# Kernel optimization log

Measured on AMD Instinct MI355X. Metric: run time of the kernel, lower is better.

The kernel has to match this reference:

```python
import jax, jax.numpy as jnp
import numpy as np

B, S, D = 256, 256, 1024
P = D // 2  # proj_dim default = input_dim / 2
NUM_HIDDEN = 2
EPS = 1e-7  # K.epsilon()
INIT_SCALE = 0.05  # keras 'uniform' init


def setup_inputs() -> dict:
    key = jax.random.key(0)
    ks = jax.random.split(key, 8)
    x = jax.random.normal(ks[0], (B, S, D), dtype=jnp.float32)
    mask = jax.random.randint(ks[1], (B, S), 0, 2).astype(bool)
    u = lambda k, shp: jax.random.uniform(k, shp, jnp.float32, -INIT_SCALE, INIT_SCALE)
    proj_head = u(ks[2], (D, P))
    proj_prep = u(ks[3], (D, P))
    proj_child = u(ks[4], (D, P))
    hidden_layers = u(ks[5], (NUM_HIDDEN, P, P))
    scorer = u(ks[6], (P,))
    return {"x": x, "proj_head": proj_head, "proj_prep": proj_prep,
            "proj_child": proj_child, "hidden_layers": hidden_layers,
            "scorer": scorer, "mask": mask}


def reference(x, proj_head, proj_prep, proj_child, hidden_layers, scorer, mask):
    # x: [B, S, D]; last two timesteps are preposition and child noun.
    head_enc = x[:, :-2, :]          # [B, S-2, D]
    prep_enc = x[:, -2, :]           # [B, D]
    child_enc = x[:, -1, :]          # [B, D]

    head_proj = jnp.einsum('bsd,dp->bsp', head_enc, proj_head)      # [B, S-2, P]
    prep_proj = (prep_enc @ proj_prep)[:, None, :]                  # [B, 1, P]
    child_proj = (child_enc @ proj_child)[:, None, :]               # [B, 1, P]

    # composition_type == 'HPCT'
    composed = jnp.tanh(head_proj + prep_proj + child_proj)         # [B, S-2, P]

    for i in range(hidden_layers.shape[0]):  # small fixed layer count
        composed = jnp.tanh(jnp.einsum('bsp,pq->bsq', composed, hidden_layers[i]))

    scores = jnp.einsum('bsp,p->bs', composed, scorer)              # [B, S-2]

    # masked exp-normalization (as in the original Keras code)
    exp_scores = jnp.exp(scores)
    head_mask = mask[:, :-2]
    masked_exp = jnp.where(head_mask, exp_scores, 0.0)
    exp_sum = jnp.sum(masked_exp, axis=1, keepdims=True) + EPS
    return masked_exp / exp_sum
```

## Files before the change

kernel.cpp:

```cpp
#include <hip/hip_runtime.h>
#include <hip/hip_bf16.h>
#include <stdint.h>

#define B_ 256
#define S_ 256
#define D_ 1024
#define P_ 512
#define SH 254
#define M_ (B_*SH)
#define EPSF 1e-7f

typedef __attribute__((ext_vector_type(8))) short short8v;
typedef __attribute__((ext_vector_type(4))) float float4v;

__device__ inline short f2bf(float f) {
  __hip_bfloat16 h = __float2bfloat16(f);
  return *reinterpret_cast<short*>(&h);
}
__device__ inline float fast_tanh(float x) {
  float e = __expf(2.0f * x);
  return 1.0f - 2.0f * __builtin_amdgcn_rcpf(e + 1.0f);
}

__global__ void k_detect(const unsigned char* m, int* flag) {
  __shared__ int c0, c3;
  if (threadIdx.x == 0) { c0 = 0; c3 = 0; }
  __syncthreads();
  int f0 = 0, f3 = 0;
  for (int i = threadIdx.x; i < 4096; i += 256) {
    unsigned char v = m[i];
    if (v != 0) {
      if ((i & 3) == 0) f0 = 1;
      if ((i & 3) == 3) f3 = 1;
    }
  }
  if (f0) atomicOr(&c0, 1);
  if (f3) atomicOr(&c3, 1);
  __syncthreads();
  if (threadIdx.x == 0) {
    int f;
    if (c3 == 0) f = 0;
    else if (c0 != 0) f = 1;
    else f = 2;
    *flag = f;
  }
}

__global__ void k_trans_head(const float* w, short* out) {
  int idx = blockIdx.x * 256 + threadIdx.x;
  int n = idx & (P_ - 1);
  int k = idx >> 9;
  out[(k >> 5) * (P_*32) + n*32 + (k & 31)] = f2bf(w[k*P_ + n]);
}

__global__ void k_trans_hidden(const float* h, short* o0, short* o1) {
  int idx = blockIdx.x * 256 + threadIdx.x;
  int which = idx >> 18;
  int j = idx & ((P_*P_) - 1);
  int n = j & (P_ - 1);
  int k = j >> 9;
  short v = f2bf(h[which*(P_*P_) + k*P_ + n]);
  short* o = which ? o1 : o0;
  o[(k >> 5) * (P_*32) + n*32 + (k & 31)] = v;
}

__global__ void __launch_bounds__(512) k_pc(const float* __restrict__ x,
                                            const float* __restrict__ wp,
                                            const float* __restrict__ wc,
                                            float* __restrict__ pc) {
  __shared__ float xs[16][256];
  int bg = blockIdx.x >> 4, cs = blockIdx.x & 15;
  int t = threadIdx.x;
  int bloc = t >> 5, c = t & 31;
  int batch = bg * 16 + bloc;
  int col = cs * 32 + c;
  float acc = 0.f;
  #pragma unroll
  for (int half = 0; half < 2; half++) {
    const float* wsrc = half ? wc : wp;
    for (int kc = 0; kc < 4; kc++) {
      const float* xr = x + ((size_t)(batch * S_ + SH + half)) * D_ + kc*256 + c*8;
      float4 v0 = *(const float4*)(xr + 0);
      float4 v1 = *(const float4*)(xr + 4);
      __syncthreads();
      *(float4*)&xs[bloc][c*8 + 0] = v0;
      *(float4*)&xs[bloc][c*8 + 4] = v1;
      __syncthreads();
      const float* wv = wsrc + (size_t)(kc*256) * P_ + col;
      #pragma unroll 8
      for (int d = 0; d < 256; d++) {
        acc += xs[bloc][d] * wv[(size_t)d * P_];
      }
    }
  }
  pc[batch * P_ + col] = acc;
}

__global__ void __launch_bounds__(512, 2) k_main(
    const float* __restrict__ x, const short* __restrict__ wth,
    const short* __restrict__ h0t, const short* __restrict__ h1t,
    const float* __restrict__ scorer, const float* __restrict__ pc,
    float* __restrict__ scores)
{
  __shared__ __attribute__((aligned(16))) short As[2][64*136];
  __shared__ __attribute__((aligned(16))) short Cs[64*520];
  __shared__ float scorer_s[P_];
  __shared__ float score_s[64];

  const int tid  = threadIdx.x;
  const int lane = tid & 63;
  const int wn   = tid >> 6;
  const int l15  = lane & 15, quad = lane >> 4;
  const int rowbase = blockIdx.x * 64;

  scorer_s[tid] = scorer[tid];
  if (tid < 64) score_s[tid] = 0.f;

  const int arow = tid >> 3;
  const int akg  = (tid & 7) * 16;
  {
    int r0 = rowbase + arow;
    int ab = r0 / SH;
    int as_ = r0 - ab * SH;
    const float* aptr = x + ((size_t)(ab * S_ + as_)) * D_ + akg;

    float4 st0 = *(const float4*)(aptr + 0);
    float4 st1 = *(const float4*)(aptr + 4);
    float4 st2 = *(const float4*)(aptr + 8);
    float4 st3 = *(const float4*)(aptr + 12);
    short8v s0 = { f2bf(st0.x),f2bf(st0.y),f2bf(st0.z),f2bf(st0.w),
                   f2bf(st1.x),f2bf(st1.y),f2bf(st1.z),f2bf(st1.w) };
    short8v s1 = { f2bf(st2.x),f2bf(st2.y),f2bf(st2.z),f2bf(st2.w),
                   f2bf(st3.x),f2bf(st3.y),f2bf(st3.z),f2bf(st3.w) };
    *(short8v*)&As[0][arow*136 + akg]     = s0;
    *(short8v*)&As[0][arow*136 + akg + 8] = s1;
    __syncthreads();

    float4v acc[4][4];
    #pragma unroll
    for (int i = 0; i < 4; i++)
      #pragma unroll
      for (int j = 0; j < 4; j++) acc[i][j] = (float4v){0.f,0.f,0.f,0.f};

    const uint4* wb = (const uint4*)wth;

    for (int sc = 0; sc < 8; sc++) {
      const int cur = sc & 1;
      float4 n0, n1, n2, n3;
      if (sc < 7) {
        const float* p = aptr + (sc + 1) * 128;
        n0 = *(const float4*)(p + 0);
        n1 = *(const float4*)(p + 4);
        n2 = *(const float4*)(p + 8);
        n3 = *(const float4*)(p + 12);
      }
      #pragma unroll
      for (int c = 0; c < 4; c++) {
        const int kc = sc * 4 + c;
        short8v a[4];
        #pragma unroll
        for (int mt = 0; mt < 4; mt++)
          a[mt] = *(const short8v*)&As[cur][(mt*16 + l15)*136 + c*32 + quad*8];
        #pragma unroll
        for (int nt = 0; nt < 4; nt++) {
          uint4 bv = wb[(size_t)kc*2048 + (wn*64 + nt*16 + l15)*4 + quad];
          short8v bfr = *(short8v*)&bv;
          #pragma unroll
          for (int mt = 0; mt < 4; mt++)
            acc[mt][nt] = __builtin_amdgcn_mfma_f32_16x16x32_bf16(a[mt], bfr, acc[mt][nt], 0, 0, 0);
        }
      }
      if (sc < 7) {
        short8v w0 = { f2bf(n0.x),f2bf(n0.y),f2bf(n0.z),f2bf(n0.w),
                       f2bf(n1.x),f2bf(n1.y),f2bf(n1.z),f2bf(n1.w) };
        short8v w1 = { f2bf(n2.x),f2bf(n2.y),f2bf(n2.z),f2bf(n2.w),
                       f2bf(n3.x),f2bf(n3.y),f2bf(n3.z),f2bf(n3.w) };
        *(short8v*)&As[cur ^ 1][arow*136 + akg]     = w0;
        *(short8v*)&As[cur ^ 1][arow*136 + akg + 8] = w1;
      }
      __syncthreads();
    }

    #pragma unroll
    for (int mt = 0; mt < 4; mt++) {
      #pragma unroll
      for (int j = 0; j < 4; j++) {
        int rl = mt*16 + quad*4 + j;
        int rg = rowbase + rl;
        int bb = rg / SH;
        const float* pcb = pc + bb * P_;
        #pragma unroll
        for (int nt = 0; nt < 4; nt++) {
          int col = wn*64 + nt*16 + l15;
          float v = fast_tanh(acc[mt][nt][j] + pcb[col]);
          float o = __shfl_xor(v, 1, 64);
          unsigned hs = (unsigned short)f2bf(v);
          unsigned ho = (unsigned short)f2bf(o);
          if ((l15 & 1) == 0)
            *(unsigned*)&Cs[rl*520 + col] = hs | (ho << 16);
        }
      }
    }
    __syncthreads();

    #pragma unroll 1
    for (int stage = 0; stage < 2; stage++) {
      const uint4* hb = (const uint4*)(stage ? h1t : h0t);
      #pragma unroll
      for (int i = 0; i < 4; i++)
        #pragma unroll
        for (int j = 0; j < 4; j++) acc[i][j] = (float4v){0.f,0.f,0.f,0.f};
      #pragma unroll 4
      for (int kc = 0; kc < 16; kc++) {
        short8v a[4];
        #pragma unroll
        for (int mt = 0; mt < 4; mt++)
          a[mt] = *(const short8v*)&Cs[(mt*16 + l15)*520 + kc*32 + quad*8];
        #pragma unroll
        for (int nt = 0; nt < 4; nt++) {
          uint4 bv = hb[(size_t)kc*2048 + (wn*64 + nt*16 + l15)*4 + quad];
          short8v bfr = *(short8v*)&bv;
          #pragma unroll
          for (int mt = 0; mt < 4; mt++)
            acc[mt][nt] = __builtin_amdgcn_mfma_f32_16x16x32_bf16(a[mt], bfr, acc[mt][nt], 0, 0, 0);
        }
      }
      if (stage == 0) {
        __syncthreads();
        #pragma unroll
        for (int mt = 0; mt < 4; mt++) {
          #pragma unroll
          for (int j = 0; j < 4; j++) {
            int rl = mt*16 + quad*4 + j;
            #pragma unroll
            for (int nt = 0; nt < 4; nt++) {
              int col = wn*64 + nt*16 + l15;
              float v = fast_tanh(acc[mt][nt][j]);
              float o = __shfl_xor(v, 1, 64);
              unsigned hs = (unsigned short)f2bf(v);
              unsigned ho = (unsigned short)f2bf(o);
              if ((l15 & 1) == 0)
                *(unsigned*)&Cs[rl*520 + col] = hs | (ho << 16);
            }
          }
        }
        __syncthreads();
      }
    }

    #pragma unroll
    for (int mt = 0; mt < 4; mt++) {
      #pragma unroll
      for (int j = 0; j < 4; j++) {
        float part = 0.f;
        #pragma unroll
        for (int nt = 0; nt < 4; nt++) {
          int col = wn*64 + nt*16 + l15;
          part += fast_tanh(acc[mt][nt][j]) * scorer_s[col];
        }
        #pragma unroll
        for (int o = 1; o < 16; o <<= 1) part += __shfl_xor(part, o, 64);
        if (l15 == 0) atomicAdd(&score_s[mt*16 + quad*4 + j], part);
      }
    }
  }
  __syncthreads();
  if (tid < 64) scores[rowbase + tid] = __expf(score_s[tid]);
}

__global__ void __launch_bounds__(256) k_softmax(const float* __restrict__ scores,
                                                 const void* __restrict__ mask,
                                                 const int* __restrict__ flag,
                                                 float* __restrict__ out) {
  int b = blockIdx.x, t = threadIdx.x;
  int lane = t & 63, w = t >> 6;
  __shared__ float ps[4];
  float me = 0.f;
  bool valid = t < SH;
  if (valid) {
    float e = scores[b*SH + t];
    int f = *flag;
    bool mb;
    if (f == 1)      mb = ((const unsigned char*)mask)[b*S_ + t] != 0;
    else if (f == 2) mb = ((const float*)mask)[b*S_ + t] != 0.0f;
    else             mb = ((const int*)mask)[b*S_ + t] != 0;
    me = mb ? e : 0.f;
  }
  float v = me;
  for (int o = 1; o < 64; o <<= 1) v += __shfl_xor(v, o, 64);
  if (lane == 0) ps[w] = v;
  __syncthreads();
  float tot = ps[0] + ps[1] + ps[2] + ps[3] + EPSF;
  if (valid) out[b*SH + t] = me / tot;
}

extern "C" void kernel_launch(void* const* d_in, const int* in_sizes, int n_in,
                              void* d_out, int out_size, void* d_ws, size_t ws_size,
                              hipStream_t stream) {
  const float* x          = (const float*)d_in[0];
  const float* proj_head  = (const float*)d_in[1];
  const float* proj_prep  = (const float*)d_in[2];
  const float* proj_child = (const float*)d_in[3];
  const float* hidden     = (const float*)d_in[4];
  const float* scorer     = (const float*)d_in[5];
  const void*  mask       = d_in[6];
  float* out = (float*)d_out;
  char* ws = (char*)d_ws;

  int*   flag   = (int*)  (ws + 0);
  float* pc     = (float*)(ws + 256);
  short* wth    = (short*)(ws + 524544);
  short* h0t    = (short*)(ws + 1573120);
  short* h1t    = (short*)(ws + 2097408);
  float* scores = (float*)(ws + 2621696);

  k_detect<<<1, 256, 0, stream>>>((const unsigned char*)mask, flag);
  k_trans_head<<<2048, 256, 0, stream>>>(proj_head, wth);
  k_trans_hidden<<<2048, 256, 0, stream>>>(hidden, h0t, h1t);
  k_pc<<<256, 512, 0, stream>>>(x, proj_prep, proj_child, pc);
  k_main<<<1016, 512, 0, stream>>>(x, wth, h0t, h1t, scorer, pc, scores);
  k_softmax<<<256, 256, 0, stream>>>(scores, mask, flag, out);
}
```

Baseline: 745.5 us.

## Prefetch B fragments into registers, cache pc in LDS, drop score atomics

The main kernel now software-pipelines weight-fragment loads into two register buffers, prefetching the next pair of K-chunks while MFMAs run on the current pair. The prefetch carries across the stage boundary into the second hidden layer. The per-batch pc rows are staged in shared memory, and the LDS atomicAdd score reduction is replaced by per-wave slots summed at the end. The transpose kernels now write packed pairs of bf16 values. The double buffers add register pressure, which under the 512x2 launch bounds risks spills.

```diff
diff --git a/kernel.cpp b/kernel.cpp
--- a/kernel.cpp
+++ b/kernel.cpp
@@ -46,22 +46,33 @@
   }
 }
 
-__global__ void k_trans_head(const float* w, short* out) {
+__global__ void k_trans_head(const float* __restrict__ w, short* __restrict__ out) {
   int idx = blockIdx.x * 256 + threadIdx.x;
-  int n = idx & (P_ - 1);
-  int k = idx >> 9;
-  out[(k >> 5) * (P_*32) + n*32 + (k & 31)] = f2bf(w[k*P_ + n]);
-}
-
-__global__ void k_trans_hidden(const float* h, short* o0, short* o1) {
+  int kc  = idx >> 13;
+  int j   = idx & 8191;
+  int krp = j >> 9;
+  int n   = j & 511;
+  int k0  = kc * 32 + krp * 2;
+  unsigned lo = (unsigned short)f2bf(w[(size_t)k0 * P_ + n]);
+  unsigned hi = (unsigned short)f2bf(w[(size_t)(k0 + 1) * P_ + n]);
+  ((unsigned*)out)[kc * 8192 + n * 16 + krp] = lo | (hi << 16);
+}
+
+__global__ void k_trans_hidden(const float* __restrict__ h,
+                               short* __restrict__ o0, short* __restrict__ o1) {
   int idx = blockIdx.x * 256 + threadIdx.x;
-  int which = idx >> 18;
-  int j = idx & ((P_*P_) - 1);
-  int n = j & (P_ - 1);
-  int k = j >> 9;
-  short v = f2bf(h[which*(P_*P_) + k*P_ + n]);
-  short* o = which ? o1 : o0;
-  o[(k >> 5) * (P_*32) + n*32 + (k & 31)] = v;
+  int which = idx >> 17;
+  int j = idx & 131071;
+  int kc  = j >> 13;
+  int r   = j & 8191;
+  int krp = r >> 9;
+  int n   = r & 511;
+  const float* hs = h + (size_t)which * (P_*P_);
+  int k0 = kc * 32 + krp * 2;
+  unsigned lo = (unsigned short)f2bf(hs[(size_t)k0 * P_ + n]);
+  unsigned hi = (unsigned short)f2bf(hs[(size_t)(k0 + 1) * P_ + n]);
+  unsigned* o = (unsigned*)(which ? o1 : o0);
+  o[kc * 8192 + n * 16 + krp] = lo | (hi << 16);
 }
 
 __global__ void __launch_bounds__(512) k_pc(const float* __restrict__ x,
@@ -96,6 +107,41 @@
   pc[batch * P_ + col] = acc;
 }
 
+
+#define LB2(DST, BASE, KC0) do {                                    \
+  const uint4* _p = (BASE) + (size_t)(KC0)*2048 + bcol;             \
+  DST[0]=_p[0];    DST[1]=_p[64];      DST[2]=_p[128];  DST[3]=_p[192]; \
+  DST[4]=_p[2048]; DST[5]=_p[2048+64]; DST[6]=_p[2048+128]; DST[7]=_p[2048+192]; \
+} while(0)
+
+#define APAIR(CUR, CB, BUF) do {                                    \
+  _Pragma("unroll") for (int cc = 0; cc < 2; cc++) {                \
+    short8v a_[4];                                                  \
+    _Pragma("unroll") for (int mt = 0; mt < 4; mt++)                \
+      a_[mt] = *(const short8v*)&As[CUR][(mt*16 + l15)*136 + ((CB)+cc)*32 + quad*8]; \
+    _Pragma("unroll") for (int nt = 0; nt < 4; nt++) {              \
+      short8v bfr = *(short8v*)&BUF[cc*4 + nt];                     \
+      _Pragma("unroll") for (int mt = 0; mt < 4; mt++)              \
+        acc[mt][nt] = __builtin_amdgcn_mfma_f32_16x16x32_bf16(a_[mt], bfr, acc[mt][nt], 0, 0, 0); \
+    }                                                               \
+  }                                                                 \
+} while(0)
+
+#define S23(P, CURB, NXTB) do {                                     \
+  if ((P) < 7) { LB2(NXTB, hb, 2*(P)+2); }                          \
+  else if (stage == 0) { LB2(NXTB, h1v, 0); }                       \
+  _Pragma("unroll") for (int cc = 0; cc < 2; cc++) {                \
+    short8v a_[4];                                                  \
+    _Pragma("unroll") for (int mt = 0; mt < 4; mt++)                \
+      a_[mt] = *(const short8v*)&Cs[(mt*16 + l15)*520 + (2*(P)+cc)*32 + quad*8]; \
+    _Pragma("unroll") for (int nt = 0; nt < 4; nt++) {              \
+      short8v bfr = *(short8v*)&CURB[cc*4 + nt];                    \
+      _Pragma("unroll") for (int mt = 0; mt < 4; mt++)              \
+        acc[mt][nt] = __builtin_amdgcn_mfma_f32_16x16x32_bf16(a_[mt], bfr, acc[mt][nt], 0, 0, 0); \
+    }                                                               \
+  }                                                                 \
+} while(0)
+
 __global__ void __launch_bounds__(512, 2) k_main(
     const float* __restrict__ x, const short* __restrict__ wth,
     const short* __restrict__ h0t, const short* __restrict__ h1t,
@@ -105,7 +151,8 @@
   __shared__ __attribute__((aligned(16))) short As[2][64*136];
   __shared__ __attribute__((aligned(16))) short Cs[64*520];
   __shared__ float scorer_s[P_];
-  __shared__ float score_s[64];
+  __shared__ float pcs[2][P_];
+  __shared__ float score_ws[64][8];
 
   const int tid  = threadIdx.x;
   const int lane = tid & 63;
@@ -114,16 +161,27 @@
   const int rowbase = blockIdx.x * 64;
 
   scorer_s[tid] = scorer[tid];
-  if (tid < 64) score_s[tid] = 0.f;
+  const int bb0 = rowbase / SH;
+  const int bb1 = (rowbase + 63) / SH;
+  pcs[0][tid] = pc[bb0 * P_ + tid];
+  pcs[1][tid] = pc[bb1 * P_ + tid];
+  const int lim1 = (bb0 + 1) * SH;
 
   const int arow = tid >> 3;
   const int akg  = (tid & 7) * 16;
+  int r0 = rowbase + arow;
+  int ab = r0 / SH;
+  int as_ = r0 - ab * SH;
+  const float* aptr = x + ((size_t)(ab * S_ + as_)) * D_ + akg;
+
+  const uint4* wbv = (const uint4*)wth;
+  const uint4* h0v = (const uint4*)h0t;
+  const uint4* h1v = (const uint4*)h1t;
+  const int bcol = (wn*64 + l15)*4 + quad;
+
+  uint4 bA[8], bB[8];
+
   {
-    int r0 = rowbase + arow;
-    int ab = r0 / SH;
-    int as_ = r0 - ab * SH;
-    const float* aptr = x + ((size_t)(ab * S_ + as_)) * D_ + akg;
-
     float4 st0 = *(const float4*)(aptr + 0);
     float4 st1 = *(const float4*)(aptr + 4);
     float4 st2 = *(const float4*)(aptr + 8);
@@ -134,138 +192,122 @@
                    f2bf(st3.x),f2bf(st3.y),f2bf(st3.z),f2bf(st3.w) };
     *(short8v*)&As[0][arow*136 + akg]     = s0;
     *(short8v*)&As[0][arow*136 + akg + 8] = s1;
+  }
+  LB2(bA, wbv, 0);
+  __syncthreads();
+
+  float4v acc[4][4];
+  #pragma unroll
+  for (int i = 0; i < 4; i++)
+    #pragma unroll
+    for (int j = 0; j < 4; j++) acc[i][j] = (float4v){0.f,0.f,0.f,0.f};
+
+  for (int sc = 0; sc < 8; sc++) {
+    const int cur = sc & 1;
+    float4 n0, n1, n2, n3;
+    if (sc < 7) {
+      const float* p = aptr + (sc + 1) * 128;
+      n0 = *(const float4*)(p + 0);
+      n1 = *(const float4*)(p + 4);
+      n2 = *(const float4*)(p + 8);
+      n3 = *(const float4*)(p + 12);
+    }
+    LB2(bB, wbv, 4*sc + 2);
+    APAIR(cur, 0, bA);
+    if (sc < 7) { LB2(bA, wbv, 4*sc + 4); }
+    APAIR(cur, 2, bB);
+    if (sc < 7) {
+      short8v w0 = { f2bf(n0.x),f2bf(n0.y),f2bf(n0.z),f2bf(n0.w),
+                     f2bf(n1.x),f2bf(n1.y),f2bf(n1.z),f2bf(n1.w) };
+      short8v w1 = { f2bf(n2.x),f2bf(n2.y),f2bf(n2.z),f2bf(n2.w),
+                     f2bf(n3.x),f2bf(n3.y),f2bf(n3.z),f2bf(n3.w) };
+      *(short8v*)&As[cur ^ 1][arow*136 + akg]     = w0;
+      *(short8v*)&As[cur ^ 1][arow*136 + akg + 8] = w1;
+    }
     __syncthreads();
-
-    float4v acc[4][4];
+  }
+
+  LB2(bA, h0v, 0);
+
+  #pragma unroll
+  for (int mt = 0; mt < 4; mt++) {
+    #pragma unroll
+    for (int j = 0; j < 4; j++) {
+      int rl = mt*16 + quad*4 + j;
+      int rg = rowbase + rl;
+      const float* pcb = (rg >= lim1) ? pcs[1] : pcs[0];
+      #pragma unroll
+      for (int nt = 0; nt < 4; nt++) {
+        int col = wn*64 + nt*16 + l15;
+        float v = fast_tanh(acc[mt][nt][j] + pcb[col]);
+        float o = __shfl_xor(v, 1, 64);
+        unsigned hs = (unsigned short)f2bf(v);
+        unsigned ho = (unsigned short)f2bf(o);
+        if ((l15 & 1) == 0)
+          *(unsigned*)&Cs[rl*520 + col] = hs | (ho << 16);
+      }
+    }
+  }
+  __syncthreads();
+
+  #pragma unroll 1
+  for (int stage = 0; stage < 2; stage++) {
+    const uint4* hb = stage ? h1v : h0v;
     #pragma unroll
     for (int i = 0; i < 4; i++)
       #pragma unroll
       for (int j = 0; j < 4; j++) acc[i][j] = (float4v){0.f,0.f,0.f,0.f};
 
-    const uint4* wb = (const uint4*)wth;
-
-    for (int sc = 0; sc < 8; sc++) {
-      const int cur = sc & 1;
-      float4 n0, n1, n2, n3;
-      if (sc < 7) {
-        const float* p = aptr + (sc + 1) * 128;
-        n0 = *(const float4*)(p + 0);
-        n1 = *(const float4*)(p + 4);
-        n2 = *(const float4*)(p + 8);
-        n3 = *(const float4*)(p + 12);
-      }
-      #pragma unroll
-      for (int c = 0; c < 4; c++) {
-        const int kc = sc * 4 + c;
-        short8v a[4];
+    S23(0, bA, bB); S23(1, bB, bA);
+    S23(2, bA, bB); S23(3, bB, bA);
+    S23(4, bA, bB); S23(5, bB, bA);
+    S23(6, bA, bB); S23(7, bB, bA);
+
+    if (stage == 0) {
+      __syncthreads();
+      #pragma unroll
+      for (int mt = 0; mt < 4; mt++) {
         #pragma unroll
-        for (int mt = 0; mt < 4; mt++)
-          a[mt] = *(const short8v*)&As[cur][(mt*16 + l15)*136 + c*32 + quad*8];
-        #pragma unroll
-        for (int nt = 0; nt < 4; nt++) {
-          uint4 bv = wb[(size_t)kc*2048 + (wn*64 + nt*16 + l15)*4 + quad];
-          short8v bfr = *(short8v*)&bv;
+        for (int j = 0; j < 4; j++) {
+          int rl = mt*16 + quad*4 + j;
           #pragma unroll
-          for (int mt = 0; mt < 4; mt++)
-            acc[mt][nt] = __builtin_amdgcn_mfma_f32_16x16x32_bf16(a[mt], bfr, acc[mt][nt], 0, 0, 0);
+          for (int nt = 0; nt < 4; nt++) {
+            int col = wn*64 + nt*16 + l15;
+            float v = fast_tanh(acc[mt][nt][j]);
+            float o = __shfl_xor(v, 1, 64);
+            unsigned hs = (unsigned short)f2bf(v);
+            unsigned ho = (unsigned short)f2bf(o);
+            if ((l15 & 1) == 0)
+              *(unsigned*)&Cs[rl*520 + col] = hs | (ho << 16);
+          }
         }
       }
-      if (sc < 7) {
-        short8v w0 = { f2bf(n0.x),f2bf(n0.y),f2bf(n0.z),f2bf(n0.w),
-                       f2bf(n1.x),f2bf(n1.y),f2bf(n1.z),f2bf(n1.w) };
-        short8v w1 = { f2bf(n2.x),f2bf(n2.y),f2bf(n2.z),f2bf(n2.w),
-                       f2bf(n3.x),f2bf(n3.y),f2bf(n3.z),f2bf(n3.w) };
-        *(short8v*)&As[cur ^ 1][arow*136 + akg]     = w0;
-        *(short8v*)&As[cur ^ 1][arow*136 + akg + 8] = w1;
+      __syncthreads();
+    }
+  }
+
+  #pragma unroll
+  for (int mt = 0; mt < 4; mt++) {
+    #pragma unroll
+    for (int j = 0; j < 4; j++) {
+      float part = 0.f;
+      #pragma unroll
+      for (int nt = 0; nt < 4; nt++) {
+        int col = wn*64 + nt*16 + l15;
+        part += fast_tanh(acc[mt][nt][j]) * scorer_s[col];
       }
-      __syncthreads();
-    }
-
-    #pragma unroll
-    for (int mt = 0; mt < 4; mt++) {
-      #pragma unroll
-      for (int j = 0; j < 4; j++) {
-        int rl = mt*16 + quad*4 + j;
-        int rg = rowbase + rl;
-        int bb = rg / SH;
-        const float* pcb = pc + bb * P_;
-        #pragma unroll
-        for (int nt = 0; nt < 4; nt++) {
-          int col = wn*64 + nt*16 + l15;
-          float v = fast_tanh(acc[mt][nt][j] + pcb[col]);
-          float o = __shfl_xor(v, 1, 64);
-          unsigned hs = (unsigned short)f2bf(v);
-          unsigned ho = (unsigned short)f2bf(o);
-          if ((l15 & 1) == 0)
-            *(unsigned*)&Cs[rl*520 + col] = hs | (ho << 16);
-        }
-      }
-    }
-    __syncthreads();
-
-    #pragma unroll 1
-    for (int stage = 0; stage < 2; stage++) {
-      const uint4* hb = (const uint4*)(stage ? h1t : h0t);
-      #pragma unroll
-      for (int i = 0; i < 4; i++)
-        #pragma unroll
-        for (int j = 0; j < 4; j++) acc[i][j] = (float4v){0.f,0.f,0.f,0.f};
-      #pragma unroll 4
-      for (int kc = 0; kc < 16; kc++) {
-        short8v a[4];
-        #pragma unroll
-        for (int mt = 0; mt < 4; mt++)
-          a[mt] = *(const short8v*)&Cs[(mt*16 + l15)*520 + kc*32 + quad*8];
-        #pragma unroll
-        for (int nt = 0; nt < 4; nt++) {
-          uint4 bv = hb[(size_t)kc*2048 + (wn*64 + nt*16 + l15)*4 + quad];
-          short8v bfr = *(short8v*)&bv;
-          #pragma unroll
-          for (int mt = 0; mt < 4; mt++)
-            acc[mt][nt] = __builtin_amdgcn_mfma_f32_16x16x32_bf16(a[mt], bfr, acc[mt][nt], 0, 0, 0);
-        }
-      }
-      if (stage == 0) {
-        __syncthreads();
-        #pragma unroll
-        for (int mt = 0; mt < 4; mt++) {
-          #pragma unroll
-          for (int j = 0; j < 4; j++) {
-            int rl = mt*16 + quad*4 + j;
-            #pragma unroll
-            for (int nt = 0; nt < 4; nt++) {
-              int col = wn*64 + nt*16 + l15;
-              float v = fast_tanh(acc[mt][nt][j]);
-              float o = __shfl_xor(v, 1, 64);
-              unsigned hs = (unsigned short)f2bf(v);
-              unsigned ho = (unsigned short)f2bf(o);
-              if ((l15 & 1) == 0)
-                *(unsigned*)&Cs[rl*520 + col] = hs | (ho << 16);
-            }
-          }
-        }
-        __syncthreads();
-      }
-    }
-
-    #pragma unroll
-    for (int mt = 0; mt < 4; mt++) {
-      #pragma unroll
-      for (int j = 0; j < 4; j++) {
-        float part = 0.f;
-        #pragma unroll
-        for (int nt = 0; nt < 4; nt++) {
-          int col = wn*64 + nt*16 + l15;
-          part += fast_tanh(acc[mt][nt][j]) * scorer_s[col];
-        }
-        #pragma unroll
-        for (int o = 1; o < 16; o <<= 1) part += __shfl_xor(part, o, 64);
-        if (l15 == 0) atomicAdd(&score_s[mt*16 + quad*4 + j], part);
-      }
-    }
-  }
-  __syncthreads();
-  if (tid < 64) scores[rowbase + tid] = __expf(score_s[tid]);
+      #pragma unroll
+      for (int o = 1; o < 16; o <<= 1) part += __shfl_xor(part, o, 64);
+      if (l15 == 0) score_ws[mt*16 + quad*4 + j][wn] = part;
+    }
+  }
+  __syncthreads();
+  if (tid < 64) {
+    float s = 0.f;
+    #pragma unroll
+    for (int k = 0; k < 8; k++) s += score_ws[tid][k];
+    scores[rowbase + tid] = __expf(s);
+  }
 }
 
 __global__ void __launch_bounds__(256) k_softmax(const float* __restrict__ scores,
@@ -315,8 +357,8 @@
   float* scores = (float*)(ws + 2621696);
 
   k_detect<<<1, 256, 0, stream>>>((const unsigned char*)mask, flag);
-  k_trans_head<<<2048, 256, 0, stream>>>(proj_head, wth);
-  k_trans_hidden<<<2048, 256, 0, stream>>>(hidden, h0t, h1t);
+  k_trans_head<<<1024, 256, 0, stream>>>(proj_head, wth);
+  k_trans_hidden<<<1024, 256, 0, stream>>>(hidden, h0t, h1t);
   k_pc<<<256, 512, 0, stream>>>(x, proj_prep, proj_child, pc);
   k_main<<<1016, 512, 0, stream>>>(x, wth, h0t, h1t, scorer, pc, scores);
   k_softmax<<<256, 256, 0, stream>>>(scores, mask, flag, out);
```

Result: faster. 695.3 us (-6.7%).
